# Optimization experiments

Hardware: AMD Instinct MI355X
Metric: run time of the kernel (lower is better)

The kernel has to match this reference:

```python
import jax, jax.numpy as jnp
import numpy as np

EMA = 0.999
EPS = 1e-8


def setup_inputs() -> dict:
    key = jax.random.key(0)
    k1, k2, k3 = jax.random.split(key, 3)
    B, z_dim, H, W = 16, 64, 32, 32
    M = 4096
    N = B * H * W
    return {
        "z": jax.random.normal(k1, (B, z_dim, H, W), dtype=jnp.float32),
        "e": jax.random.normal(k2, (M, z_dim), dtype=jnp.float32),
        "belong": jax.random.uniform(k3, (N, M), dtype=jnp.float32),
        "log_sigma": jnp.zeros((1,), dtype=jnp.float32),
        "max_distance": jnp.ones((1, M), dtype=jnp.float32),
        "distance_p": 2,
    }


def reference(z, e, belong, log_sigma, max_distance, distance_p):
    B, z_dim, H, W = z.shape
    # [B, z_dim, H, W] -> [N, z_dim], N = B*H*W
    zf = jnp.transpose(z, (0, 2, 3, 1)).reshape(-1, z_dim)
    # pairwise L2 distance via GEMM expansion: ||z||^2 + ||e||^2 - 2 z.e
    d2 = (jnp.sum(zf * zf, axis=1, keepdims=True)
          + jnp.sum(e * e, axis=1)[None, :]
          - 2.0 * (zf @ e.T))                      # [N, M]
    distance = jnp.sqrt(jnp.maximum(d2, 0.0))
    # EMA update of per-code max distance (buffer, no grad in original)
    batch_max = jnp.max(belong * distance, axis=0, keepdims=True)  # [1, M]
    new_max = EMA * max_distance + (1.0 - EMA) * batch_max
    new_max = jax.lax.stop_gradient(jnp.clip(new_max, EPS, None))
    p = float(distance_p)
    distance = jnp.where(distance < new_max,
                         distance ** (2.0 / p),
                         distance ** (2.0 * p))
    alpha = -1.0 / (2.0 * jnp.exp(log_sigma) ** 2)  # shape (1,)
    lse = jax.scipy.special.logsumexp(alpha * distance, axis=0)  # [M]
    loss = -jnp.mean(lse) + z_dim * log_sigma  # shape (1,), as in torch
    return loss
```

## Files before the change

### kernel.cpp

```cpp
#include <hip/hip_runtime.h>
#include <hip/hip_bf16.h>

#define ZD    64
#define MM    4096
#define NN    16384
#define HWSZ  1024
#define BB    16
#define NPART 128

typedef __bf16 bf16x8 __attribute__((ext_vector_type(8)));
typedef float  f32x4  __attribute__((ext_vector_type(4)));

#define EMA_C 0.999f
#define EPS_C 1e-8f

__global__ __launch_bounds__(256) void k_prep(const float* __restrict__ z,
                                              const float* __restrict__ e,
                                              __hip_bfloat16* __restrict__ zf,
                                              __hip_bfloat16* __restrict__ ebf,
                                              float* __restrict__ zn2,
                                              float* __restrict__ en2,
                                              float* __restrict__ sume) {
    __shared__ float tile[64][65];
    __shared__ float part[4][64];
    int blk = blockIdx.x;
    int tid = threadIdx.x;
    if (blk < 256) {
        int b   = blk >> 4;
        int hw0 = (blk & 15) * 64;
        int tx = tid & 63, ty = tid >> 6;
        const float* zp = z + (size_t)b * (ZD * HWSZ);
#pragma unroll
        for (int kk = 0; kk < 16; kk++) {
            int k = kk * 4 + ty;
            tile[k][tx] = zp[(size_t)k * HWSZ + hw0 + tx];
        }
        __syncthreads();
#pragma unroll
        for (int i = 0; i < 16; i++) {
            int li = tid + i * 256;
            int ln = li >> 6, lk = li & 63;
            int n = b * HWSZ + hw0 + ln;
            zf[(size_t)n * ZD + lk] = __float2bfloat16(tile[lk][ln]);
        }
        float s = 0.f;
#pragma unroll
        for (int kk = 0; kk < 16; kk++) {
            float q = __bfloat162float(__float2bfloat16(tile[ty + kk * 4][tx]));
            s += q * q;
        }
        part[ty][tx] = s;
        __syncthreads();
        if (tid < 64) {
            float t = part[0][tid] + part[1][tid] + part[2][tid] + part[3][tid];
            zn2[b * HWSZ + hw0 + tid] = t;
        }
    } else {
        int eb  = blk - 256;
        int gid = eb * 256 + tid;
        if (gid < MM) sume[gid] = 0.f;
        int wave = tid >> 6, lane = tid & 63;
        int row = eb * 4 + wave;
        if (row < MM) {
            float v = e[row * ZD + lane];
            __hip_bfloat16 b16 = __float2bfloat16(v);
            ebf[row * ZD + lane] = b16;
            float q = __bfloat162float(b16);
            float s = q * q;
            for (int off = 32; off; off >>= 1) s += __shfl_xor(s, off);
            if (lane == 0) en2[row] = s;
        }
    }
}

__global__ __launch_bounds__(256) void k_pass1(const __hip_bfloat16* __restrict__ zf,
                                               const __hip_bfloat16* __restrict__ ebf,
                                               const float* __restrict__ zn2,
                                               const float* __restrict__ en2,
                                               const float* __restrict__ belong,
                                               float* __restrict__ pmax,
                                               float* __restrict__ pmin) {
    int tid = threadIdx.x;
    int wave = tid >> 6, lane = tid & 63;
    int l16 = lane & 15, lq = lane >> 4;
    int wm = wave & 1, wn = wave >> 1;
    int m0 = blockIdx.x * 64 + wm * 32;
    int n0 = blockIdx.y * 128 + wn * 64;

    const bf16x8* ebv = reinterpret_cast<const bf16x8*>(ebf);
    const bf16x8* zfv = reinterpret_cast<const bf16x8*>(zf);

    bf16x8 Af[2][2], Bf[4][2];
#pragma unroll
    for (int im = 0; im < 2; im++)
#pragma unroll
        for (int h = 0; h < 2; h++)
            Af[im][h] = ebv[(size_t)(m0 + im * 16 + l16) * 8 + h * 4 + lq];
#pragma unroll
    for (int jn = 0; jn < 4; jn++)
#pragma unroll
        for (int h = 0; h < 2; h++)
            Bf[jn][h] = zfv[(size_t)(n0 + jn * 16 + l16) * 8 + h * 4 + lq];

    f32x4 bl[2][4];
#pragma unroll
    for (int im = 0; im < 2; im++)
#pragma unroll
        for (int jn = 0; jn < 4; jn++) {
            const f32x4* bp = reinterpret_cast<const f32x4*>(
                belong + (size_t)(n0 + jn * 16 + l16) * MM + (m0 + im * 16 + lq * 4));
            bl[im][jn] = __builtin_nontemporal_load(bp);
        }

    f32x4 acc[2][4];
#pragma unroll
    for (int im = 0; im < 2; im++)
#pragma unroll
        for (int jn = 0; jn < 4; jn++) {
            acc[im][jn] = (f32x4){0.f, 0.f, 0.f, 0.f};
            acc[im][jn] = __builtin_amdgcn_mfma_f32_16x16x32_bf16(Af[im][0], Bf[jn][0], acc[im][jn], 0, 0, 0);
            acc[im][jn] = __builtin_amdgcn_mfma_f32_16x16x32_bf16(Af[im][1], Bf[jn][1], acc[im][jn], 0, 0, 0);
        }

    f32x4 en2v[2];
#pragma unroll
    for (int im = 0; im < 2; im++)
        en2v[im] = *reinterpret_cast<const f32x4*>(en2 + m0 + im * 16 + lq * 4);
    float zn2v[4];
#pragma unroll
    for (int jn = 0; jn < 4; jn++)
        zn2v[jn] = zn2[n0 + jn * 16 + l16];

    float vmax[2][4], vmin[2][4];
#pragma unroll
    for (int im = 0; im < 2; im++)
#pragma unroll
        for (int r = 0; r < 4; r++) { vmax[im][r] = 0.f; vmin[im][r] = 3.4e38f; }

#pragma unroll
    for (int im = 0; im < 2; im++)
#pragma unroll
        for (int jn = 0; jn < 4; jn++)
#pragma unroll
            for (int r = 0; r < 4; r++) {
                float d2  = fmaf(-2.f, acc[im][jn][r], en2v[im][r] + zn2v[jn]);
                float bel = bl[im][jn][r];
                vmax[im][r] = fmaxf(vmax[im][r], bel * bel * d2);
                vmin[im][r] = fminf(vmin[im][r], d2);
            }

#pragma unroll
    for (int off = 1; off < 16; off <<= 1)
#pragma unroll
        for (int im = 0; im < 2; im++)
#pragma unroll
            for (int r = 0; r < 4; r++) {
                vmax[im][r] = fmaxf(vmax[im][r], __shfl_xor(vmax[im][r], off));
                vmin[im][r] = fminf(vmin[im][r], __shfl_xor(vmin[im][r], off));
            }

    __shared__ unsigned smax[64];
    __shared__ float    smin2[2][64];
    if (tid < 64) smax[tid] = 0u;
    __syncthreads();
    if (l16 == 0) {
#pragma unroll
        for (int im = 0; im < 2; im++)
#pragma unroll
            for (int r = 0; r < 4; r++) {
                int ml = wm * 32 + im * 16 + lq * 4 + r;
                atomicMax(&smax[ml], __float_as_uint(fmaxf(vmax[im][r], 0.f)));
                smin2[wn][ml] = vmin[im][r];
            }
    }
    __syncthreads();
    if (tid < 64) {
        int m = blockIdx.x * 64 + tid;
        pmax[(size_t)blockIdx.y * MM + m] = __uint_as_float(smax[tid]);
        pmin[(size_t)blockIdx.y * MM + m] = fminf(smin2[0][tid], smin2[1][tid]);
    }
}

__global__ __launch_bounds__(256) void k_pass2(const __hip_bfloat16* __restrict__ zf,
                                               const __hip_bfloat16* __restrict__ ebf,
                                               const float* __restrict__ zn2,
                                               const float* __restrict__ en2,
                                               const float* __restrict__ pmax,
                                               const float* __restrict__ pmin,
                                               const float* __restrict__ max_distance,
                                               const float* __restrict__ log_sigma,
                                               const int* __restrict__ pp,
                                               float* __restrict__ refs,
                                               float* __restrict__ sume) {
    __shared__ float sred[256];
    __shared__ float snm2[128], sref[128], ssum[128];
    int tid = threadIdx.x;

    int p = pp[0];
    float alpha = -0.5f * __expf(-2.f * log_sigma[0]);

    {
        int half = tid >> 7;
        int col  = tid & 127;
        int m    = blockIdx.y * 128 + col;
        const float* base = (half ? pmin : pmax) + m;
        float a0 = half ? 3.4e38f : 0.f;
#pragma unroll 8
        for (int yp = 0; yp < NPART; yp++) {
            float v = base[(size_t)yp * MM];
            a0 = half ? fminf(a0, v) : fmaxf(a0, v);
        }
        sred[tid] = a0;
    }
    __syncthreads();
    if (tid < 128) {
        int m = blockIdx.y * 128 + tid;
        float bm = sqrtf(fmaxf(sred[tid], 0.f));
        float dm = sqrtf(fmaxf(sred[tid + 128], 0.f));
        float nm = fmaxf(EMA_C * max_distance[m] + (1.f - EMA_C) * bm, EPS_C);
        float tlow;
        if (p == 2) {
            float d4  = (dm * dm) * (dm * dm);
            float nm4 = (nm * nm) * (nm * nm);
            tlow = (dm < nm) ? fminf(dm, nm4) : d4;
        } else {
            float e1 = 2.f / (float)p, e2 = 2.f * (float)p;
            tlow = (dm < nm) ? fminf(powf(dm, e1), powf(nm, e2)) : powf(dm, e2);
        }
        float rf = alpha * tlow;
        snm2[tid] = nm * nm;
        sref[tid] = rf;
        ssum[tid] = 0.f;
        if (blockIdx.x == 0) refs[m] = rf;
    }
    __syncthreads();

    int wave = tid >> 6, lane = tid & 63;
    int l16 = lane & 15, lq = lane >> 4;
    int wn = wave >> 1, wm = wave & 1;
    int n0 = blockIdx.x * 64 + wn * 32;
    int m0 = blockIdx.y * 128 + wm * 64;

    const bf16x8* zfv = reinterpret_cast<const bf16x8*>(zf);
    const bf16x8* ebv = reinterpret_cast<const bf16x8*>(ebf);

    bf16x8 Af[2][2], Bf[4][2];
#pragma unroll
    for (int i = 0; i < 2; i++)
#pragma unroll
        for (int h = 0; h < 2; h++)
            Af[i][h] = zfv[(size_t)(n0 + i * 16 + l16) * 8 + h * 4 + lq];
#pragma unroll
    for (int j = 0; j < 4; j++)
#pragma unroll
        for (int h = 0; h < 2; h++)
            Bf[j][h] = ebv[(size_t)(m0 + j * 16 + l16) * 8 + h * 4 + lq];

    f32x4 acc[2][4];
#pragma unroll
    for (int i = 0; i < 2; i++)
#pragma unroll
        for (int j = 0; j < 4; j++) {
            acc[i][j] = (f32x4){0.f, 0.f, 0.f, 0.f};
            acc[i][j] = __builtin_amdgcn_mfma_f32_16x16x32_bf16(Af[i][0], Bf[j][0], acc[i][j], 0, 0, 0);
            acc[i][j] = __builtin_amdgcn_mfma_f32_16x16x32_bf16(Af[i][1], Bf[j][1], acc[i][j], 0, 0, 0);
        }

    f32x4 zn2v[2];
#pragma unroll
    for (int i = 0; i < 2; i++)
        zn2v[i] = *reinterpret_cast<const f32x4*>(zn2 + n0 + i * 16 + lq * 4);

    bool p2 = (p == 2);
    float pe = (float)p, pi = 1.f / (float)p;

#pragma unroll
    for (int j = 0; j < 4; j++) {
        float en2v = en2[m0 + j * 16 + l16];
        float nm2v = snm2[wm * 64 + j * 16 + l16];
        float rfv  = sref[wm * 64 + j * 16 + l16];
        float csum = 0.f;
#pragma unroll
        for (int i = 0; i < 2; i++)
#pragma unroll
            for (int r = 0; r < 4; r++) {
                float d2c = fmaxf(zn2v[i][r] + en2v - 2.f * acc[i][j][r], 0.f);
                float t;
                if (p2) {
                    t = d2c * d2c;
                    if (__any(d2c < nm2v))
                        t = (d2c < nm2v) ? sqrtf(d2c) : t;
                } else {
                    t = powf(d2c, (d2c < nm2v) ? pi : pe);
                }
                csum += __expf(fmaf(alpha, t, -rfv));
            }
        csum += __shfl_xor(csum, 16);
        csum += __shfl_xor(csum, 32);
        if (lane < 16) atomicAdd(&ssum[wm * 64 + j * 16 + lane], csum);
    }
    __syncthreads();
    if (tid < 128) atomicAdd(&sume[blockIdx.y * 128 + tid], ssum[tid]);
}

__global__ __launch_bounds__(256) void k_final(const float* __restrict__ refs,
                                               const float* __restrict__ sume,
                                               const float* __restrict__ log_sigma,
                                               float* __restrict__ out) {
    __shared__ float red[4];
    int tid = threadIdx.x;
    float a = 0.f;
    for (int m = tid; m < MM; m += 256)
        a += refs[m] + logf(fmaxf(sume[m], 1e-30f));
    for (int off = 32; off; off >>= 1) a += __shfl_xor(a, off);
    int wave = tid >> 6, lane = tid & 63;
    if (lane == 0) red[wave] = a;
    __syncthreads();
    if (tid == 0) {
        float t = red[0] + red[1] + red[2] + red[3];
        out[0] = -t / (float)MM + (float)ZD * log_sigma[0];
    }
}

extern "C" void kernel_launch(void* const* d_in, const int* in_sizes, int n_in,
                              void* d_out, int out_size, void* d_ws, size_t ws_size,
                              hipStream_t stream) {
    const float* z            = (const float*)d_in[0];
    const float* e            = (const float*)d_in[1];
    const float* belong       = (const float*)d_in[2];
    const float* log_sigma    = (const float*)d_in[3];
    const float* max_distance = (const float*)d_in[4];
    const int*   pp           = (const int*)d_in[5];
    float* out = (float*)d_out;

    char* ws = (char*)d_ws;
    __hip_bfloat16* zf  = (__hip_bfloat16*)(ws + 0);
    __hip_bfloat16* ebf = (__hip_bfloat16*)(ws + 2097152);
    float* zn2  = (float*)(ws + 2621440);
    float* en2  = (float*)(ws + 2686976);
    float* pmax = (float*)(ws + 2703360);
    float* pmin = (float*)(ws + 4800512);
    float* refs = (float*)(ws + 6897664);
    float* sume = (float*)(ws + 6914048);

    k_prep<<<1280, 256, 0, stream>>>(z, e, zf, ebf, zn2, en2, sume);
    k_pass1<<<dim3(MM / 64, NN / 128), 256, 0, stream>>>(zf, ebf, zn2, en2, belong, pmax, pmin);
    k_pass2<<<dim3(NN / 64, MM / 128), 256, 0, stream>>>(zf, ebf, zn2, en2, pmax, pmin,
                                                         max_distance, log_sigma, pp, refs, sume);
    k_final<<<1, 256, 0, stream>>>(refs, sume, log_sigma, out);
}
```

Before: 561.3 us.

## Hoist per-code partial max/min reduction into separate mid kernel

```diff
diff --git a/kernel.cpp b/kernel.cpp
--- a/kernel.cpp
+++ b/kernel.cpp
@@ -181,43 +181,34 @@
     }
 }
 
-__global__ __launch_bounds__(256) void k_pass2(const __hip_bfloat16* __restrict__ zf,
-                                               const __hip_bfloat16* __restrict__ ebf,
-                                               const float* __restrict__ zn2,
-                                               const float* __restrict__ en2,
-                                               const float* __restrict__ pmax,
-                                               const float* __restrict__ pmin,
-                                               const float* __restrict__ max_distance,
-                                               const float* __restrict__ log_sigma,
-                                               const int* __restrict__ pp,
-                                               float* __restrict__ refs,
-                                               float* __restrict__ sume) {
-    __shared__ float sred[256];
-    __shared__ float snm2[128], sref[128], ssum[128];
-    int tid = threadIdx.x;
-
-    int p = pp[0];
-    float alpha = -0.5f * __expf(-2.f * log_sigma[0]);
-
-    {
-        int half = tid >> 7;
-        int col  = tid & 127;
-        int m    = blockIdx.y * 128 + col;
-        const float* base = (half ? pmin : pmax) + m;
-        float a0 = half ? 3.4e38f : 0.f;
+__global__ __launch_bounds__(256) void k_mid(const float* __restrict__ pmax,
+                                             const float* __restrict__ pmin,
+                                             const float* __restrict__ max_distance,
+                                             const float* __restrict__ log_sigma,
+                                             const int* __restrict__ pp,
+                                             float* __restrict__ nm2,
+                                             float* __restrict__ refs) {
+    __shared__ float sx[4][64], sn[4][64];
+    int tid = threadIdx.x;
+    int col = tid & 63, grp = tid >> 6;
+    int m = blockIdx.x * 64 + col;
+    float vmax = 0.f, vmin = 3.4e38f;
 #pragma unroll 8
-        for (int yp = 0; yp < NPART; yp++) {
-            float v = base[(size_t)yp * MM];
-            a0 = half ? fminf(a0, v) : fmaxf(a0, v);
-        }
-        sred[tid] = a0;
-    }
-    __syncthreads();
-    if (tid < 128) {
-        int m = blockIdx.y * 128 + tid;
-        float bm = sqrtf(fmaxf(sred[tid], 0.f));
-        float dm = sqrtf(fmaxf(sred[tid + 128], 0.f));
-        float nm = fmaxf(EMA_C * max_distance[m] + (1.f - EMA_C) * bm, EPS_C);
+    for (int yp = grp * (NPART / 4); yp < (grp + 1) * (NPART / 4); yp++) {
+        vmax = fmaxf(vmax, pmax[(size_t)yp * MM + m]);
+        vmin = fminf(vmin, pmin[(size_t)yp * MM + m]);
+    }
+    sx[grp][col] = vmax;
+    sn[grp][col] = vmin;
+    __syncthreads();
+    if (tid < 64) {
+        float bx = fmaxf(fmaxf(sx[0][tid], sx[1][tid]), fmaxf(sx[2][tid], sx[3][tid]));
+        float dn = fminf(fminf(sn[0][tid], sn[1][tid]), fminf(sn[2][tid], sn[3][tid]));
+        int mm = blockIdx.x * 64 + tid;
+        float bm = sqrtf(fmaxf(bx, 0.f));
+        float dm = sqrtf(fmaxf(dn, 0.f));
+        float nm = fmaxf(EMA_C * max_distance[mm] + (1.f - EMA_C) * bm, EPS_C);
+        int p = pp[0];
         float tlow;
         if (p == 2) {
             float d4  = (dm * dm) * (dm * dm);
@@ -227,11 +218,31 @@
             float e1 = 2.f / (float)p, e2 = 2.f * (float)p;
             tlow = (dm < nm) ? fminf(powf(dm, e1), powf(nm, e2)) : powf(dm, e2);
         }
-        float rf = alpha * tlow;
-        snm2[tid] = nm * nm;
-        sref[tid] = rf;
+        float alpha = -0.5f * __expf(-2.f * log_sigma[0]);
+        nm2[mm]  = nm * nm;
+        refs[mm] = alpha * tlow;
+    }
+}
+
+__global__ __launch_bounds__(256) void k_pass2(const __hip_bfloat16* __restrict__ zf,
+                                               const __hip_bfloat16* __restrict__ ebf,
+                                               const float* __restrict__ zn2,
+                                               const float* __restrict__ en2,
+                                               const float* __restrict__ nm2,
+                                               const float* __restrict__ refsg,
+                                               const float* __restrict__ log_sigma,
+                                               const int* __restrict__ pp,
+                                               float* __restrict__ sume) {
+    __shared__ float snm2[128], sref[128], ssum[128];
+    int tid = threadIdx.x;
+    int p = pp[0];
+    float alpha = -0.5f * __expf(-2.f * log_sigma[0]);
+
+    if (tid < 128) {
+        int m = blockIdx.y * 128 + tid;
+        snm2[tid] = nm2[m];
+        sref[tid] = refsg[m];
         ssum[tid] = 0.f;
-        if (blockIdx.x == 0) refs[m] = rf;
     }
     __syncthreads();
 
@@ -286,13 +297,8 @@
             for (int r = 0; r < 4; r++) {
                 float d2c = fmaxf(zn2v[i][r] + en2v - 2.f * acc[i][j][r], 0.f);
                 float t;
-                if (p2) {
-                    t = d2c * d2c;
-                    if (__any(d2c < nm2v))
-                        t = (d2c < nm2v) ? sqrtf(d2c) : t;
-                } else {
-                    t = powf(d2c, (d2c < nm2v) ? pi : pe);
-                }
+                if (p2) t = (d2c < nm2v) ? sqrtf(d2c) : d2c * d2c;
+                else    t = powf(d2c, (d2c < nm2v) ? pi : pe);
                 csum += __expf(fmaf(alpha, t, -rfv));
             }
         csum += __shfl_xor(csum, 16);
@@ -340,12 +346,14 @@
     float* en2  = (float*)(ws + 2686976);
     float* pmax = (float*)(ws + 2703360);
     float* pmin = (float*)(ws + 4800512);
-    float* refs = (float*)(ws + 6897664);
-    float* sume = (float*)(ws + 6914048);
+    float* nm2  = (float*)(ws + 6897664);
+    float* refs = (float*)(ws + 6914048);
+    float* sume = (float*)(ws + 6930432);
 
     k_prep<<<1280, 256, 0, stream>>>(z, e, zf, ebf, zn2, en2, sume);
     k_pass1<<<dim3(MM / 64, NN / 128), 256, 0, stream>>>(zf, ebf, zn2, en2, belong, pmax, pmin);
-    k_pass2<<<dim3(NN / 64, MM / 128), 256, 0, stream>>>(zf, ebf, zn2, en2, pmax, pmin,
-                                                         max_distance, log_sigma, pp, refs, sume);
+    k_mid<<<MM / 64, 256, 0, stream>>>(pmax, pmin, max_distance, log_sigma, pp, nm2, refs);
+    k_pass2<<<dim3(NN / 64, MM / 128), 256, 0, stream>>>(zf, ebf, zn2, en2, nm2, refs,
+                                                         log_sigma, pp, sume);
     k_final<<<1, 256, 0, stream>>>(refs, sume, log_sigma, out);
 }
```

Result: faster. 494.7 us (-11.9%).
